# Optimization experiments

Hardware: AMD Instinct MI355X
Metric: run time of the kernel (lower is better)

Reference implementation:

```python
import jax, jax.numpy as jnp
import numpy as np

N_NODES = 100000
N_EDGES = 1600000
IN_F = 256
OUT_F = 64


def setup_inputs() -> dict:
    key = jax.random.key(0)
    k1, k2, k3, k4, k5 = jax.random.split(key, 5)
    features = jax.random.normal(k1, (N_NODES, IN_F), dtype=jnp.float32)
    # xavier_uniform for [in, out] weight
    limit = float(np.sqrt(6.0 / (IN_F + OUT_F)))
    weight = jax.random.uniform(k2, (IN_F, OUT_F), dtype=jnp.float32, minval=-limit, maxval=limit)
    adj_rows = jnp.sort(jax.random.randint(k3, (N_EDGES,), 0, N_NODES, dtype=jnp.int32))
    adj_cols = jax.random.randint(k4, (N_EDGES,), 0, N_NODES, dtype=jnp.int32)
    # positive edge weights (e.g. normalized adjacency values)
    adj_vals = jax.random.uniform(k5, (N_EDGES,), dtype=jnp.float32) * (1.0 / 16.0)
    return {
        "features": features,
        "weight": weight,
        "adj_rows": adj_rows,
        "adj_cols": adj_cols,
        "adj_vals": adj_vals,
        "active": 1,
    }


def _spmm(rows, cols, vals, x, n_nodes):
    # sparse [N,N] @ dense [N,F]: gather neighbor rows, scale, scatter-add
    gathered = vals[:, None] * x[cols]          # [E, F]
    return jax.ops.segment_sum(gathered, rows, num_segments=n_nodes)


def reference(features, weight, adj_rows, adj_cols, adj_vals, active):
    support = features @ weight                 # [N, out]
    if active:
        support = jnp.tanh(support)
    n = features.shape[0]
    output = _spmm(adj_rows, adj_cols, adj_vals, support, n)  # adj @ support
    az = _spmm(adj_rows, adj_cols, adj_vals, output, n)       # adj @ output
    return (output, az)
```

## Files before the change

kernel.cpp:

```cpp
#include <hip/hip_runtime.h>
#include <hip/hip_bf16.h>
#include <math.h>

#define IN_F  256
#define OUT_F 64
#define PD    264

typedef __attribute__((ext_vector_type(8))) short bf16x8;
typedef __attribute__((ext_vector_type(4))) float f32x4;
typedef __attribute__((ext_vector_type(2))) float f32x2;

__device__ inline unsigned short f2b(float x) {
    union { __hip_bfloat16 h; unsigned short u; } cv;
    cv.h = __float2bfloat16(x);
    return cv.u;
}
__device__ inline float b2f_lo(unsigned int u) { return __uint_as_float(u << 16); }
__device__ inline float b2f_hi(unsigned int u) { return __uint_as_float(u & 0xffff0000u); }

__global__ __launch_bounds__(512) void gemm_rowptr_kernel(
    const float* __restrict__ feat,
    const float* __restrict__ w,
    const int*  __restrict__ active,
    const int*  __restrict__ rows,
    unsigned short* __restrict__ sup_bf,
    int* __restrict__ row_ptr,
    int N, int E, int GB)
{
    __shared__ unsigned short wt[OUT_F * PD];

    if ((int)blockIdx.x >= GB) {
        int e = ((int)blockIdx.x - GB) * 512 + (int)threadIdx.x;
        if (e < E) {
            int r  = rows[e];
            int rn = (e + 1 < E) ? rows[e + 1] : N;
            if (e == 0) {
                for (int j = 0; j <= r; ++j) row_ptr[j] = 0;
            }
            for (int j = r + 1; j <= rn; ++j) row_ptr[j] = e + 1;
        }
        return;
    }

    const int t = threadIdx.x;
    #pragma unroll
    for (int r = 0; r < 8; ++r) {
        int f = r * 512 + t;
        float4 v = ((const float4*)w)[f];
        int k = f >> 4;
        int n = (f & 15) << 2;
        wt[(n + 0) * PD + k] = f2b(v.x);
        wt[(n + 1) * PD + k] = f2b(v.y);
        wt[(n + 2) * PD + k] = f2b(v.z);
        wt[(n + 3) * PD + k] = f2b(v.w);
    }
    __syncthreads();

    const int lane = t & 63;
    const int m    = lane & 15;
    const int quad = lane >> 4;
    const int node0 = (int)blockIdx.x * 128 + (t >> 6) * 16;

    int nd = node0 + m;
    if (nd > N - 1) nd = N - 1;
    const float* arow = feat + (size_t)nd * IN_F;

    f32x4 acc[4];
    #pragma unroll
    for (int b = 0; b < 4; ++b) acc[b] = (f32x4)0.0f;

    #pragma unroll
    for (int kt = 0; kt < 8; ++kt) {
        const int ko = kt * 32 + quad * 8;
        f32x4 lo = __builtin_nontemporal_load((const f32x4*)(arow + ko));
        f32x4 hi = __builtin_nontemporal_load((const f32x4*)(arow + ko + 4));
        bf16x8 a;
        a[0] = (short)f2b(lo[0]); a[1] = (short)f2b(lo[1]);
        a[2] = (short)f2b(lo[2]); a[3] = (short)f2b(lo[3]);
        a[4] = (short)f2b(hi[0]); a[5] = (short)f2b(hi[1]);
        a[6] = (short)f2b(hi[2]); a[7] = (short)f2b(hi[3]);
        #pragma unroll
        for (int nt = 0; nt < 4; ++nt) {
            bf16x8 b = *(const bf16x8*)(&wt[(nt * 16 + m) * PD + ko]);
            acc[nt] = __builtin_amdgcn_mfma_f32_16x16x32_bf16(a, b, acc[nt], 0, 0, 0);
        }
    }

    int act = __builtin_amdgcn_readfirstlane(active[0]);
    #pragma unroll
    for (int r = 0; r < 4; ++r) {
        int node = node0 + quad * 4 + r;
        if (node >= N) continue;
        #pragma unroll
        for (int nt = 0; nt < 4; ++nt) {
            float v = acc[nt][r];
            if (act) v = tanhf(v);
            sup_bf[(size_t)node * OUT_F + nt * 16 + m] = f2b(v);
        }
    }
}

__device__ inline int lower_bound(const int* __restrict__ a, int n, int key) {
    int lo = 0, hi = n;
    while (lo < hi) {
        int mid = (lo + hi) >> 1;
        if (a[mid] < key) lo = mid + 1; else hi = mid;
    }
    return lo;
}

template <bool XBF>
__global__ __launch_bounds__(256) void spmm_kernel(
    const int* __restrict__ row_ptr,
    const int* __restrict__ rows,
    const int* __restrict__ cols,
    const float* __restrict__ vals,
    const void* __restrict__ x,
    float* __restrict__ out,
    unsigned short* __restrict__ out_bf,
    int N, int E)
{
    const int lane = threadIdx.x & 63;
    const int h    = lane >> 5;
    const int l    = lane & 31;
    const int row  = blockIdx.x * 8 + (threadIdx.x >> 6) * 2 + h;

    const bool valid = row < N;
    const int  rc    = valid ? row : N - 1;

    int s, e;
    if (row_ptr) { s = row_ptr[rc]; e = row_ptr[rc + 1]; }
    else         { s = lower_bound(rows, E, rc); e = lower_bound(rows, E, rc + 1); }
    if (!valid) e = s;

    const unsigned short* xb = (const unsigned short*)x;
    const float*          xf = (const float*)x;

    float a0 = 0.0f, a1 = 0.0f;

    for (int base = s; base < e; base += 16) {
        int   c[16];
        float v[16];
        #pragma unroll
        for (int j = 0; j < 16; ++j) {
            int idx = base + j;
            int cl  = idx < e ? idx : e - 1;
            c[j] = cols[cl];
            v[j] = (idx < e) ? vals[cl] : 0.0f;
        }
        if (XBF) {
            #pragma unroll
            for (int j = 0; j < 16; ++j) {
                unsigned int g = *(const unsigned int*)(xb + (size_t)c[j] * OUT_F + 2 * l);
                a0 = fmaf(v[j], b2f_lo(g), a0);
                a1 = fmaf(v[j], b2f_hi(g), a1);
            }
        } else {
            #pragma unroll
            for (int j = 0; j < 16; ++j) {
                float2 g = *(const float2*)(xf + (size_t)c[j] * OUT_F + 2 * l);
                a0 = fmaf(v[j], g.x, a0);
                a1 = fmaf(v[j], g.y, a1);
            }
        }
    }

    if (valid) {
        size_t bidx = (size_t)row * OUT_F + 2 * l;
        f32x2 o = {a0, a1};
        __builtin_nontemporal_store(o, (f32x2*)(out + bidx));
        if (out_bf) {
            unsigned int pk = (unsigned int)f2b(a0) | ((unsigned int)f2b(a1) << 16);
            *(unsigned int*)(out_bf + bidx) = pk;
        }
    }
}

extern "C" void kernel_launch(void* const* d_in, const int* in_sizes, int n_in,
                              void* d_out, int out_size, void* d_ws, size_t ws_size,
                              hipStream_t stream) {
    const float* feat   = (const float*)d_in[0];
    const float* w      = (const float*)d_in[1];
    const int*   rows   = (const int*)d_in[2];
    const int*   cols   = (const int*)d_in[3];
    const float* vals   = (const float*)d_in[4];
    const int*   active = (const int*)d_in[5];

    const int N = in_sizes[0] / IN_F;
    const int E = in_sizes[2];

    float* out = (float*)d_out;
    float* az  = out + (size_t)N * OUT_F;

    size_t rp_bytes = (((size_t)(N + 1) * sizeof(int)) + 255) & ~(size_t)255;
    size_t bf_bytes = (((size_t)N * OUT_F * sizeof(unsigned short)) + 255) & ~(size_t)255;
    char* ws = (char*)d_ws;

    int* row_ptr = (ws_size >= rp_bytes) ? (int*)ws : nullptr;
    size_t used = row_ptr ? rp_bytes : 0;

    unsigned short* sup_bf;
    unsigned short* mid_bf = nullptr;
    if (ws_size >= used + 2 * bf_bytes) {
        sup_bf = (unsigned short*)(ws + used);
        mid_bf = (unsigned short*)(ws + used + bf_bytes);
    } else if (ws_size >= used + bf_bytes) {
        sup_bf = (unsigned short*)(ws + used);
    } else {
        sup_bf = (unsigned short*)az;
    }

    {
        int GB = (N + 127) / 128;
        int RB = row_ptr ? (E + 511) / 512 : 0;
        gemm_rowptr_kernel<<<GB + RB, 512, 0, stream>>>(
            feat, w, active, rows, sup_bf, row_ptr, N, E, GB);
    }

    int spmm_blocks = (N + 7) / 8;
    spmm_kernel<true><<<spmm_blocks, 256, 0, stream>>>(
        row_ptr, rows, cols, vals, sup_bf, out, mid_bf, N, E);
    if (mid_bf) {
        spmm_kernel<true><<<spmm_blocks, 256, 0, stream>>>(
            row_ptr, rows, cols, vals, mid_bf, az, nullptr, N, E);
    } else {
        spmm_kernel<false><<<spmm_blocks, 256, 0, stream>>>(
            row_ptr, rows, cols, vals, out, az, nullptr, N, E);
    }
}
```

Before: 263.4 us.

## Slice bf16 feature matrix by columns and map slices to XCDs for SpMM

The GEMM now writes the bf16 support matrix in a slice-major layout, four 16-column slices each stored contiguously. A new SpMM kernel assigns blocks so that each pair of XCDs handles one slice, which shrinks the gathered working set per XCD's L2. Each wave processes 8 edges at once with 8 lanes per row and reduces across lanes with shuffles. The cost is that cols and vals are re-read four times, once per slice, and every gather is a small 32-byte access. The fallback path also changes so it no longer writes a bf16 mid-result.

```diff
diff --git a/kernel.cpp b/kernel.cpp
--- a/kernel.cpp
+++ b/kernel.cpp
@@ -2,9 +2,11 @@
 #include <hip/hip_bf16.h>
 #include <math.h>
 
-#define IN_F  256
-#define OUT_F 64
-#define PD    264
+#define IN_F   256
+#define OUT_F  64
+#define NSLICE 4
+#define SLC    16
+#define PD     264
 
 typedef __attribute__((ext_vector_type(8))) short bf16x8;
 typedef __attribute__((ext_vector_type(4))) float f32x4;
@@ -25,7 +27,7 @@
     const int*  __restrict__ rows,
     unsigned short* __restrict__ sup_bf,
     int* __restrict__ row_ptr,
-    int N, int E, int GB)
+    int N, int E, int GB, int slice_major)
 {
     __shared__ unsigned short wt[OUT_F * PD];
 
@@ -95,7 +97,67 @@
         for (int nt = 0; nt < 4; ++nt) {
             float v = acc[nt][r];
             if (act) v = tanhf(v);
-            sup_bf[(size_t)node * OUT_F + nt * 16 + m] = f2b(v);
+            size_t idx = slice_major ? ((size_t)nt * N + node) * SLC + m
+                                     : (size_t)node * OUT_F + nt * 16 + m;
+            sup_bf[idx] = f2b(v);
+        }
+    }
+}
+
+template <bool HASBF>
+__global__ __launch_bounds__(256) void spmm_sliced_kernel(
+    const int* __restrict__ row_ptr,
+    const int* __restrict__ cols,
+    const float* __restrict__ vals,
+    const unsigned short* __restrict__ xs,
+    float* __restrict__ out,
+    unsigned short* __restrict__ out_bf,
+    int N)
+{
+    const int b     = blockIdx.x;
+    const int xcd   = b & 7;
+    const int slice = xcd >> 1;
+    const int sub   = (b >> 3) * 2 + (xcd & 1);
+    const int wave  = threadIdx.x >> 6;
+    const int lane  = threadIdx.x & 63;
+    const int slot  = lane >> 3;
+    const int p     = lane & 7;
+
+    const unsigned short* xsl = xs + (size_t)slice * N * SLC;
+
+    for (int rw = 0; rw < 2; ++rw) {
+        const int row = sub * 8 + wave * 2 + rw;
+        if (row >= N) return;
+        const int s = row_ptr[row], e = row_ptr[row + 1];
+
+        float a0 = 0.0f, a1 = 0.0f;
+        for (int base = s; base < e; base += 16) {
+            int ea = base + slot, eb = base + 8 + slot;
+            int ia = ea < e ? ea : e - 1;
+            int ib = eb < e ? eb : e - 1;
+            int   ca = __builtin_nontemporal_load(cols + ia);
+            int   cb = __builtin_nontemporal_load(cols + ib);
+            float va = ea < e ? __builtin_nontemporal_load(vals + ea) : 0.0f;
+            float vb = eb < e ? __builtin_nontemporal_load(vals + eb) : 0.0f;
+            unsigned int ga = *(const unsigned int*)(xsl + (size_t)ca * SLC + 2 * p);
+            unsigned int gb = *(const unsigned int*)(xsl + (size_t)cb * SLC + 2 * p);
+            a0 = fmaf(va, b2f_lo(ga), a0); a1 = fmaf(va, b2f_hi(ga), a1);
+            a0 = fmaf(vb, b2f_lo(gb), a0); a1 = fmaf(vb, b2f_hi(gb), a1);
+        }
+
+        a0 += __shfl_xor(a0, 8, 64);  a1 += __shfl_xor(a1, 8, 64);
+        a0 += __shfl_xor(a0, 16, 64); a1 += __shfl_xor(a1, 16, 64);
+        a0 += __shfl_xor(a0, 32, 64); a1 += __shfl_xor(a1, 32, 64);
+
+        if (slot == 0) {
+            size_t ob = (size_t)row * OUT_F + slice * SLC + 2 * p;
+            f32x2 o = {a0, a1};
+            __builtin_nontemporal_store(o, (f32x2*)(out + ob));
+            if (HASBF) {
+                unsigned int pk = (unsigned int)f2b(a0) | ((unsigned int)f2b(a1) << 16);
+                __builtin_nontemporal_store(pk,
+                    (unsigned int*)(out_bf + ((size_t)slice * N + row) * SLC + 2 * p));
+            }
         }
     }
 }
@@ -210,20 +272,25 @@
         sup_bf = (unsigned short*)az;
     }
 
+    const int sliced = (row_ptr && mid_bf) ? 1 : 0;
+
     {
         int GB = (N + 127) / 128;
         int RB = row_ptr ? (E + 511) / 512 : 0;
         gemm_rowptr_kernel<<<GB + RB, 512, 0, stream>>>(
-            feat, w, active, rows, sup_bf, row_ptr, N, E, GB);
-    }
-
-    int spmm_blocks = (N + 7) / 8;
-    spmm_kernel<true><<<spmm_blocks, 256, 0, stream>>>(
-        row_ptr, rows, cols, vals, sup_bf, out, mid_bf, N, E);
-    if (mid_bf) {
+            feat, w, active, rows, sup_bf, row_ptr, N, E, GB, sliced);
+    }
+
+    if (sliced) {
+        int sgrid = 8 * ((N + 15) / 16);
+        spmm_sliced_kernel<true><<<sgrid, 256, 0, stream>>>(
+            row_ptr, cols, vals, sup_bf, out, mid_bf, N);
+        spmm_sliced_kernel<false><<<sgrid, 256, 0, stream>>>(
+            row_ptr, cols, vals, mid_bf, az, nullptr, N);
+    } else {
+        int spmm_blocks = (N + 7) / 8;
         spmm_kernel<true><<<spmm_blocks, 256, 0, stream>>>(
-            row_ptr, rows, cols, vals, mid_bf, az, nullptr, N, E);
-    } else {
+            row_ptr, rows, cols, vals, sup_bf, out, nullptr, N, E);
         spmm_kernel<false><<<spmm_blocks, 256, 0, stream>>>(
             row_ptr, rows, cols, vals, out, az, nullptr, N, E);
     }
```

New measurement: 439.7 us. 1.67x slower.
